# Kernel tuning notes

Hardware: AMD Instinct MI355X
Metric: run time of the kernel (lower is better)

Reference implementation:

```python
import jax, jax.numpy as jnp
import numpy as np

H = 64       # HIDDEN_DIM
HIST = 4     # HIST_LEN
V = 64       # VOCAB_SIZE
LSTM_H = 32  # trigger LSTM hidden size


def setup_inputs() -> dict:
    key = jax.random.key(0)
    ks = jax.random.split(key, 24)
    B, L, M = 1024, 256, 256
    s = 0.1

    def p(k, shape):
        return jax.random.normal(k, shape, dtype=jnp.float32) * s

    return {
        "seq": jax.random.randint(ks[0], (B, L), 0, V, dtype=jnp.int32),
        "memory": jax.random.normal(ks[1], (B, M, H), dtype=jnp.float32),
        # nn.Embedding(V, H)
        "embed_w": p(ks[2], (V, H)),
        # nn.GRUCell(2H, H): weight_ih (3H, 2H), weight_hh (3H, H)
        "gru_wih": p(ks[3], (3 * H, 2 * H)),
        "gru_whh": p(ks[4], (3 * H, H)),
        "gru_bih": p(ks[5], (3 * H,)),
        "gru_bhh": p(ks[6], (3 * H,)),
        # SoftAttentionMemory projections: Linear(H, H) each
        "q_w": p(ks[7], (H, H)), "q_b": p(ks[8], (H,)),
        "k_w": p(ks[9], (H, H)), "k_b": p(ks[10], (H,)),
        "v_w": p(ks[11], (H, H)), "v_b": p(ks[12], (H,)),
        # PredictiveTrigger nn.LSTM(H, 32): gate order i,f,g,o
        "lstm_wih": p(ks[13], (4 * LSTM_H, H)),
        "lstm_whh": p(ks[14], (4 * LSTM_H, LSTM_H)),
        "lstm_bih": p(ks[15], (4 * LSTM_H,)),
        "lstm_bhh": p(ks[16], (4 * LSTM_H,)),
        "trig_w": p(ks[17], (1, LSTM_H)), "trig_b": p(ks[18], (1,)),
        # output head Linear(H, V)
        "head_w": p(ks[19], (V, H)), "head_b": p(ks[20], (V,)),
    }


def reference(seq, memory, embed_w, gru_wih, gru_whh, gru_bih, gru_bhh,
              q_w, q_b, k_w, k_b, v_w, v_b,
              lstm_wih, lstm_whh, lstm_bih, lstm_bhh,
              trig_w, trig_b, head_w, head_b):
    B, L = seq.shape
    x_emb = embed_w[seq]                         # (B, L, H)
    # k/v projections of memory are time-invariant -> hoist out of the loop
    kmem = memory @ k_w.T + k_b                  # (B, M, H)
    vmem = memory @ v_w.T + v_b                  # (B, M, H)
    scale = 1.0 / jnp.sqrt(jnp.float32(H))

    def gru_cell(inp, h):
        gi = inp @ gru_wih.T + gru_bih           # (B, 3H)
        gh = h @ gru_whh.T + gru_bhh
        i_r, i_z, i_n = jnp.split(gi, 3, axis=-1)
        h_r, h_z, h_n = jnp.split(gh, 3, axis=-1)
        r = jax.nn.sigmoid(i_r + h_r)
        z = jax.nn.sigmoid(i_z + h_z)
        n = jnp.tanh(i_n + r * h_n)
        return (1.0 - z) * n + z * h

    def trigger(hist):                            # hist: (B, HIST, H) -> (B,)
        def lstm_step(carry, x_t):
            hh, cc = carry
            g = x_t @ lstm_wih.T + lstm_bih + hh @ lstm_whh.T + lstm_bhh
            i, f, gg, o = jnp.split(g, 4, axis=-1)
            cc = jax.nn.sigmoid(f) * cc + jax.nn.sigmoid(i) * jnp.tanh(gg)
            hh = jax.nn.sigmoid(o) * jnp.tanh(cc)
            return (hh, cc), None
        init = (jnp.zeros((hist.shape[0], LSTM_H), hist.dtype),
                jnp.zeros((hist.shape[0], LSTM_H), hist.dtype))
        (hh, _), _ = jax.lax.scan(lstm_step, init, jnp.swapaxes(hist, 0, 1))
        return jax.nn.sigmoid(hh @ trig_w.T + trig_b)[:, 0]

    def attend(h):                                # (B, H) -> (B, H)
        q = h @ q_w.T + q_b
        w = jax.nn.softmax(jnp.einsum('bh,bmh->bm', q, kmem) * scale, axis=-1)
        return jnp.einsum('bm,bmh->bh', w, vmem)

    def step(carry, xs):
        h, retrieved, hist, reads = carry
        x_t, t = xs
        h = gru_cell(jnp.concatenate([x_t, retrieved], axis=-1), h)
        # torch uses h.detach() for the trigger history
        hist = jnp.concatenate([hist[:, 1:], jax.lax.stop_gradient(h)[:, None]], axis=1)
        full = t >= HIST - 1                      # history buffer filled
        prob = trigger(hist)
        do_read = full & (jnp.mean(prob) > 0.5)
        retrieved = jnp.where(do_read, attend(h),
                              jnp.where(full, jnp.zeros_like(retrieved), retrieved))
        reads = reads + do_read.astype(jnp.float32)
        return (h, retrieved, hist, reads), None

    carry0 = (jnp.zeros((B, H), jnp.float32),
              jnp.zeros((B, H), jnp.float32),
              jnp.zeros((B, HIST, H), jnp.float32),
              jnp.float32(0.0))
    (h, _, _, reads), _ = jax.lax.scan(step, carry0,
                                       (jnp.swapaxes(x_emb, 0, 1), jnp.arange(L)))
    logits = h @ head_w.T + head_b               # (B, V)
    read_rate = reads / L
    return logits, read_rate
```

## Files before the change

kernel.cpp:

```cpp
#include <hip/hip_runtime.h>
#include <hip/hip_fp16.h>
#include <math.h>

#define OFF_TOKPROJ 0
#define OFF_ACC     12288
#define OFF_SLOT2   12800
#define OFF_HH      78336

#define THRESH30 (512ULL << 30)
#define THRESH27 (512ULL << 27)
#define SPIN_BOUND (1 << 18)

__device__ __forceinline__ float sigf(float x) {
    return __fdividef(1.f, 1.f + __expf(-x));
}
__device__ __forceinline__ float tanhf_fast(float x) {
    float e2 = __expf(-2.f * fabsf(x));
    float r = __fdividef(1.f - e2, 1.f + e2);
    return __uint_as_float(__float_as_uint(r) | (__float_as_uint(x) & 0x80000000u));
}

__device__ __forceinline__ unsigned int pack2(float x, float y) {
    union { unsigned int u; _Float16 h[2]; } v;
    v.h[0] = (_Float16)x; v.h[1] = (_Float16)y;
    return v.u;
}
__device__ __forceinline__ float unplo(unsigned int u) {
    union { unsigned int x; _Float16 h[2]; } v; v.x = u; return (float)v.h[0];
}
__device__ __forceinline__ float unphi(unsigned int u) {
    union { unsigned int x; _Float16 h[2]; } v; v.x = u; return (float)v.h[1];
}
__device__ __forceinline__ float dot2acc(unsigned int a, unsigned int b, float acc) {
#if __has_builtin(__builtin_amdgcn_fdot2)
    typedef _Float16 hf2 __attribute__((ext_vector_type(2)));
    union { unsigned int u; hf2 h; } ua, ub;
    ua.u = a; ub.u = b;
    return __builtin_amdgcn_fdot2(ua.h, ub.h, acc, false);
#else
    union { unsigned int u; _Float16 h[2]; } ua, ub;
    ua.u = a; ub.u = b;
    return acc + (float)ua.h[0] * (float)ub.h[0] + (float)ua.h[1] * (float)ub.h[1];
#endif
}

__global__ __launch_bounds__(64) void prep_k(
    const float* __restrict__ embed, const float* __restrict__ gwih,
    const float* __restrict__ gbih, float* __restrict__ ws)
{
    int blk = blockIdx.x, l = threadIdx.x;
    if (blk < 64) {
        float* tokproj = ws + OFF_TOKPROJ;
        int v = blk;
        for (int j = l; j < 192; j += 64) {
            float s = gbih[j];
            for (int d = 0; d < 64; ++d) s += embed[v * 64 + d] * gwih[j * 128 + d];
            tokproj[v * 192 + j] = s;
        }
    } else {
        float* z = ws + OFF_ACC;
        int base = (blk - 64) * 4096;
        int end = 512 + 65536;
        for (int i = base + l; i < base + 4096; i += 64)
            if (i < end) z[i] = 0.f;
    }
}

__global__ __launch_bounds__(256, 1) void gru_k(
    const int* __restrict__ seq, const float* __restrict__ gwhh,
    const float* __restrict__ gbhh, const float* __restrict__ hw,
    const float* __restrict__ hb, float* __restrict__ ws,
    float* __restrict__ out)
{
    int tid = threadIdx.x, w = tid >> 6, l = tid & 63, b = blockIdx.x;
    int r = b * 4 + w;
    const float* tokproj = ws + OFF_TOKPROJ;
    __half* Hh = (__half*)(ws + OFF_HH);

    __shared__ float hs[4][64];
    __shared__ int toks[4][256];
    for (int k = 0; k < 4; ++k) toks[w][k * 64 + l] = seq[r * 256 + k * 64 + l];

    float wh0[64], wh1[64], wh2[64];
    #pragma unroll
    for (int d4 = 0; d4 < 16; ++d4) {
        float4 a0 = *(const float4*)(gwhh + (size_t)l * 64 + d4 * 4);
        float4 a1 = *(const float4*)(gwhh + (size_t)(64 + l) * 64 + d4 * 4);
        float4 a2 = *(const float4*)(gwhh + (size_t)(128 + l) * 64 + d4 * 4);
        wh0[d4*4] = a0.x; wh0[d4*4+1] = a0.y; wh0[d4*4+2] = a0.z; wh0[d4*4+3] = a0.w;
        wh1[d4*4] = a1.x; wh1[d4*4+1] = a1.y; wh1[d4*4+2] = a1.z; wh1[d4*4+3] = a1.w;
        wh2[d4*4] = a2.x; wh2[d4*4+1] = a2.y; wh2[d4*4+2] = a2.z; wh2[d4*4+3] = a2.w;
    }
    float g0b = gbhh[l], g1b = gbhh[64 + l], g2b = gbhh[128 + l];

    float h = 0.f;
    hs[w][l] = 0.f;
    int tok0 = toks[w][0];
    float gi0 = tokproj[tok0 * 192 + l], gi1 = tokproj[tok0 * 192 + 64 + l],
          gi2 = tokproj[tok0 * 192 + 128 + l];

    for (int t = 0; t < 256; ++t) {
        float ni0 = 0.f, ni1 = 0.f, ni2 = 0.f;
        if (t < 255) {
            int tk = toks[w][t + 1];
            ni0 = tokproj[tk * 192 + l];
            ni1 = tokproj[tk * 192 + 64 + l];
            ni2 = tokproj[tk * 192 + 128 + l];
        }
        float A0[4] = {0.f, 0.f, 0.f, 0.f};
        float A1[4] = {0.f, 0.f, 0.f, 0.f};
        float A2[4] = {0.f, 0.f, 0.f, 0.f};
        #pragma unroll
        for (int d4 = 0; d4 < 16; ++d4) {
            float4 hv = *(const float4*)&hs[w][d4 * 4];
            A0[d4 & 3] += hv.x*wh0[d4*4] + hv.y*wh0[d4*4+1] + hv.z*wh0[d4*4+2] + hv.w*wh0[d4*4+3];
            A1[d4 & 3] += hv.x*wh1[d4*4] + hv.y*wh1[d4*4+1] + hv.z*wh1[d4*4+2] + hv.w*wh1[d4*4+3];
            A2[d4 & 3] += hv.x*wh2[d4*4] + hv.y*wh2[d4*4+1] + hv.z*wh2[d4*4+2] + hv.w*wh2[d4*4+3];
        }
        float gh0 = g0b + ((A0[0] + A0[1]) + (A0[2] + A0[3]));
        float gh1 = g1b + ((A1[0] + A1[1]) + (A1[2] + A1[3]));
        float gh2 = g2b + ((A2[0] + A2[1]) + (A2[2] + A2[3]));
        float r_ = sigf(gi0 + gh0), z_ = sigf(gi1 + gh1);
        float n_ = tanhf_fast(gi2 + r_ * gh2);
        h = (1.f - z_) * n_ + z_ * h;
        hs[w][l] = h;
        Hh[((size_t)r * 256 + t) * 64 + l] = __float2half(h);
        gi0 = ni0; gi1 = ni1; gi2 = ni2;
    }

    float sL = hb[l];
    #pragma unroll
    for (int d4 = 0; d4 < 16; ++d4) {
        float4 w4 = *(const float4*)(hw + (size_t)l * 64 + d4 * 4);
        float4 hv = *(const float4*)&hs[w][d4 * 4];
        sL += hv.x * w4.x + hv.y * w4.y + hv.z * w4.z + hv.w * w4.w;
    }
    out[r * 64 + l] = sL;
}

__global__ __launch_bounds__(256) void trig_k(
    const float* __restrict__ lwih, const float* __restrict__ lwhh,
    const float* __restrict__ lbih, const float* __restrict__ lbhh,
    const float* __restrict__ tw, const float* __restrict__ tb,
    float* __restrict__ ws)
{
    int tid = threadIdx.x, w = tid >> 6, l = tid & 63, b = blockIdx.x;
    int rg = b >> 4, c = b & 15;
    int r = rg * 4 + w;
    int t0 = 3 + 16 * c;
    int ntrig = (c == 15) ? 13 : 16;
    int wlen = ntrig + 3;

    const unsigned int* HhU = (const unsigned int*)(ws + OFF_HH);
    unsigned long long* acc = (unsigned long long*)(ws + OFF_ACC);

    __shared__ unsigned int hwin2[4][608];
    __shared__ unsigned int pwinp[4][19][64];
    __shared__ unsigned int hs2p[4][2][16];
    __shared__ unsigned int probq[4][16];

    unsigned int wl0h[32], wl1h[32], lh0h[16], lh1h[16];
    #pragma unroll
    for (int d2 = 0; d2 < 32; ++d2) {
        wl0h[d2] = pack2(lwih[(size_t)l * 64 + 2*d2], lwih[(size_t)l * 64 + 2*d2 + 1]);
        wl1h[d2] = pack2(lwih[(size_t)(64 + l) * 64 + 2*d2], lwih[(size_t)(64 + l) * 64 + 2*d2 + 1]);
    }
    #pragma unroll
    for (int d2 = 0; d2 < 16; ++d2) {
        lh0h[d2] = pack2(lwhh[(size_t)l * 32 + 2*d2], lwhh[(size_t)l * 32 + 2*d2 + 1]);
        lh1h[d2] = pack2(lwhh[(size_t)(64 + l) * 32 + 2*d2], lwhh[(size_t)(64 + l) * 32 + 2*d2 + 1]);
    }
    float lb0 = lbih[l] + lbhh[l], lb1 = lbih[64 + l] + lbhh[64 + l];
    float twr = (l < 32) ? tw[l] : 0.f;
    float tb0 = tb[0];

    for (int idx = l; idx < wlen * 32; idx += 64)
        hwin2[w][idx] = HhU[((size_t)r * 256 + (t0 - 3)) * 32 + idx];

    for (int i = 0; i < wlen; ++i) {
        float p0 = lb0, p1 = lb1;
        #pragma unroll
        for (int d8 = 0; d8 < 8; ++d8) {
            uint4 hv = *(const uint4*)&hwin2[w][i * 32 + d8 * 4];
            p0 = dot2acc(hv.x, wl0h[d8*4+0], p0); p1 = dot2acc(hv.x, wl1h[d8*4+0], p1);
            p0 = dot2acc(hv.y, wl0h[d8*4+1], p0); p1 = dot2acc(hv.y, wl1h[d8*4+1], p1);
            p0 = dot2acc(hv.z, wl0h[d8*4+2], p0); p1 = dot2acc(hv.z, wl1h[d8*4+2], p1);
            p0 = dot2acc(hv.w, wl0h[d8*4+3], p0); p1 = dot2acc(hv.w, wl1h[d8*4+3], p1);
        }
        pwinp[w][i][l] = pack2(p0, p1);
    }

    for (int jp = 0; jp < 8 && jp < ntrig; ++jp) {
        int ja = jp, jb = jp + 8;
        bool hasB = (jb < ntrig);
        float hhA = 0.f, ccA = 0.f, hhB = 0.f, ccB = 0.f;
        #pragma unroll
        for (int k = 0; k < 4; ++k) {
            unsigned int uA = pwinp[w][ja + k][l];
            float q0A = unplo(uA), q1A = unphi(uA);
            float q0B = 0.f, q1B = 0.f;
            if (hasB) {
                unsigned int uB = pwinp[w][jb + k][l];
                q0B = unplo(uB); q1B = unphi(uB);
            }
            if (k) {
                #pragma unroll
                for (int d4 = 0; d4 < 4; ++d4) {
                    uint4 ha = *(const uint4*)&hs2p[w][0][d4 * 4];
                    q0A = dot2acc(ha.x, lh0h[d4*4+0], q0A); q1A = dot2acc(ha.x, lh1h[d4*4+0], q1A);
                    q0A = dot2acc(ha.y, lh0h[d4*4+1], q0A); q1A = dot2acc(ha.y, lh1h[d4*4+1], q1A);
                    q0A = dot2acc(ha.z, lh0h[d4*4+2], q0A); q1A = dot2acc(ha.z, lh1h[d4*4+2], q1A);
                    q0A = dot2acc(ha.w, lh0h[d4*4+3], q0A); q1A = dot2acc(ha.w, lh1h[d4*4+3], q1A);
                }
                if (hasB) {
                    #pragma unroll
                    for (int d4 = 0; d4 < 4; ++d4) {
                        uint4 hb2 = *(const uint4*)&hs2p[w][1][d4 * 4];
                        q0B = dot2acc(hb2.x, lh0h[d4*4+0], q0B); q1B = dot2acc(hb2.x, lh1h[d4*4+0], q1B);
                        q0B = dot2acc(hb2.y, lh0h[d4*4+1], q0B); q1B = dot2acc(hb2.y, lh1h[d4*4+1], q1B);
                        q0B = dot2acc(hb2.z, lh0h[d4*4+2], q0B); q1B = dot2acc(hb2.z, lh1h[d4*4+2], q1B);
                        q0B = dot2acc(hb2.w, lh0h[d4*4+3], q0B); q1B = dot2acc(hb2.w, lh1h[d4*4+3], q1B);
                    }
                }
            }
            float s0A = sigf(q0A);
            float t1A = tanhf_fast(q1A);
            float s1A = sigf(q1A);
            float ffA = __shfl(s0A, l + 32);
            float ooA = __shfl(s1A, l + 32);
            float nccA = ffA * ccA + s0A * t1A;
            float nhA = ooA * tanhf_fast(nccA);
            if (l < 32) { ccA = nccA; hhA = nhA; }
            float nhB = 0.f;
            if (hasB) {
                float s0B = sigf(q0B);
                float t1B = tanhf_fast(q1B);
                float s1B = sigf(q1B);
                float ffB = __shfl(s0B, l + 32);
                float ooB = __shfl(s1B, l + 32);
                float nccB = ffB * ccB + s0B * t1B;
                nhB = ooB * tanhf_fast(nccB);
                if (l < 32) { ccB = nccB; hhB = nhB; }
            }
            if (k < 3) {
                float a0 = __shfl(nhA, 2 * l), a1 = __shfl(nhA, 2 * l + 1);
                if (l < 16) hs2p[w][0][l] = pack2(a0, a1);
                if (hasB) {
                    float b0 = __shfl(nhB, 2 * l), b1 = __shfl(nhB, 2 * l + 1);
                    if (l < 16) hs2p[w][1][l] = pack2(b0, b1);
                }
            }
        }
        float ppA = (l < 32) ? hhA * twr : 0.f;
        #pragma unroll
        for (int o = 32; o; o >>= 1) ppA += __shfl_xor(ppA, o);
        if (l == 0) {
            float prob = sigf(ppA + tb0);
            unsigned long long q = (unsigned long long)llrint((double)prob * 1073741824.0);
            if (q > 0x3FFFFFFFull) q = 0x3FFFFFFFull;
            probq[w][ja] = (unsigned int)q;
        }
        if (hasB) {
            float ppB = (l < 32) ? hhB * twr : 0.f;
            #pragma unroll
            for (int o = 32; o; o >>= 1) ppB += __shfl_xor(ppB, o);
            if (l == 0) {
                float prob = sigf(ppB + tb0);
                unsigned long long q = (unsigned long long)llrint((double)prob * 1073741824.0);
                if (q > 0x3FFFFFFFull) q = 0x3FFFFFFFull;
                probq[w][jb] = (unsigned int)q;
            }
        }
    }
    __syncthreads();
    if (w == 0 && l < ntrig) {
        unsigned int s = probq[0][l] + probq[1][l] + probq[2][l] + probq[3][l];
        atomicAdd(&acc[t0 + l], (unsigned long long)s);
    }
}

__global__ __launch_bounds__(256, 1) void fin_k(
    const int* __restrict__ seq, const float* __restrict__ memory,
    const float* __restrict__ gwih, const float* __restrict__ gwhh,
    const float* __restrict__ gbhh, const float* __restrict__ qw,
    const float* __restrict__ qb, const float* __restrict__ kw,
    const float* __restrict__ vw, const float* __restrict__ vb,
    const float* __restrict__ lwih, const float* __restrict__ lwhh,
    const float* __restrict__ lbih, const float* __restrict__ lbhh,
    const float* __restrict__ tw, const float* __restrict__ tb,
    const float* __restrict__ hw, const float* __restrict__ hb,
    float* __restrict__ ws, float* __restrict__ out)
{
    int tid = threadIdx.x, w = tid >> 6, l = tid & 63, b = blockIdx.x;
    const unsigned long long* acc = (const unsigned long long*)(ws + OFF_ACC);

    __shared__ int redmin[4];
    {
        int mymin = 1 << 30;
        if (tid >= 3 && acc[tid] > THRESH30) mymin = tid;
        #pragma unroll
        for (int o = 32; o; o >>= 1) mymin = min(mymin, __shfl_xor(mymin, o));
        if (l == 0) redmin[w] = mymin;
    }
    __syncthreads();
    int tc = min(min(redmin[0], redmin[1]), min(redmin[2], redmin[3]));
    if (tc > 255) {
        if (b == 0 && tid == 0) out[65536] = 0.f;
        return;
    }

    int r = b * 4 + w;
    const float* tokproj = ws + OFF_TOKPROJ;
    unsigned int* S2 = (unsigned int*)(ws + OFF_SLOT2);

    __shared__ float hs[4][64], qs[4][64], us[4][64], rs[4][64];
    __shared__ float hs2f[4][32];
    __shared__ float PXl[4][4][128];
    __shared__ unsigned int probq[4];
    __shared__ int flagLds;
    __shared__ int toks[4][256];

    for (int k = 0; k < 4; ++k) toks[w][k * 64 + l] = seq[r * 256 + k * 64 + l];
    if (tid == 0) flagLds = 0;

    float wh0[64], wh1[64], wh2[64], wl0[64], wl1[64], lh0[32], lh1[32];
    #pragma unroll
    for (int d4 = 0; d4 < 16; ++d4) {
        float4 a0 = *(const float4*)(gwhh + (size_t)l * 64 + d4 * 4);
        float4 a1 = *(const float4*)(gwhh + (size_t)(64 + l) * 64 + d4 * 4);
        float4 a2 = *(const float4*)(gwhh + (size_t)(128 + l) * 64 + d4 * 4);
        float4 b0 = *(const float4*)(lwih + (size_t)l * 64 + d4 * 4);
        float4 b1 = *(const float4*)(lwih + (size_t)(64 + l) * 64 + d4 * 4);
        wh0[d4*4] = a0.x; wh0[d4*4+1] = a0.y; wh0[d4*4+2] = a0.z; wh0[d4*4+3] = a0.w;
        wh1[d4*4] = a1.x; wh1[d4*4+1] = a1.y; wh1[d4*4+2] = a1.z; wh1[d4*4+3] = a1.w;
        wh2[d4*4] = a2.x; wh2[d4*4+1] = a2.y; wh2[d4*4+2] = a2.z; wh2[d4*4+3] = a2.w;
        wl0[d4*4] = b0.x; wl0[d4*4+1] = b0.y; wl0[d4*4+2] = b0.z; wl0[d4*4+3] = b0.w;
        wl1[d4*4] = b1.x; wl1[d4*4+1] = b1.y; wl1[d4*4+2] = b1.z; wl1[d4*4+3] = b1.w;
    }
    #pragma unroll
    for (int d4 = 0; d4 < 8; ++d4) {
        float4 c0 = *(const float4*)(lwhh + (size_t)l * 32 + d4 * 4);
        float4 c1 = *(const float4*)(lwhh + (size_t)(64 + l) * 32 + d4 * 4);
        lh0[d4*4] = c0.x; lh0[d4*4+1] = c0.y; lh0[d4*4+2] = c0.z; lh0[d4*4+3] = c0.w;
        lh1[d4*4] = c1.x; lh1[d4*4+1] = c1.y; lh1[d4*4+2] = c1.z; lh1[d4*4+3] = c1.w;
    }
    float g0b = gbhh[l], g1b = gbhh[64 + l], g2b = gbhh[128 + l];
    float lb0 = lbih[l] + lbhh[l], lb1 = lbih[64 + l] + lbhh[64 + l];
    float twr = (l < 32) ? tw[l] : 0.f;
    float tb0 = tb[0];
    const float* mrow = memory + (size_t)r * 16384;

    float h = 0.f;
    hs[w][l] = 0.f;
    bool fire = false, brk = false;
    int cnt = 1;
    __syncthreads();

    for (int t = 0; t < 256; ++t) {
        int tok = toks[w][t];
        float gi0 = tokproj[tok * 192 + l], gi1 = tokproj[tok * 192 + 64 + l],
              gi2 = tokproj[tok * 192 + 128 + l];
        float gh0 = g0b, gh1 = g1b, gh2 = g2b;
        #pragma unroll
        for (int d4 = 0; d4 < 16; ++d4) {
            float4 hv = *(const float4*)&hs[w][d4 * 4];
            gh0 += hv.x*wh0[d4*4] + hv.y*wh0[d4*4+1] + hv.z*wh0[d4*4+2] + hv.w*wh0[d4*4+3];
            gh1 += hv.x*wh1[d4*4] + hv.y*wh1[d4*4+1] + hv.z*wh1[d4*4+2] + hv.w*wh1[d4*4+3];
            gh2 += hv.x*wh2[d4*4] + hv.y*wh2[d4*4+1] + hv.z*wh2[d4*4+2] + hv.w*wh2[d4*4+3];
        }
        if (fire) {
            float q = qb[l];
            #pragma unroll
            for (int d4 = 0; d4 < 16; ++d4) {
                float4 q4 = *(const float4*)(qw + (size_t)l * 64 + d4 * 4);
                float4 hv = *(const float4*)&hs[w][d4 * 4];
                q += hv.x * q4.x + hv.y * q4.y + hv.z * q4.z + hv.w * q4.w;
            }
            qs[w][l] = q;
            float qk = 0.f;
            for (int e = 0; e < 64; ++e) qk += qs[w][e] * kw[(size_t)e * 64 + l];
            qk *= 0.125f;
            us[w][l] = qk;
            float sc[4];
            for (int k = 0; k < 4; ++k) {
                const float* mp = mrow + (size_t)(k * 64 + l) * 64;
                float s = 0.f;
                #pragma unroll
                for (int d4 = 0; d4 < 16; ++d4) {
                    float4 m4 = *(const float4*)(mp + d4 * 4);
                    float4 kv = *(const float4*)&us[w][d4 * 4];
                    s += m4.x * kv.x + m4.y * kv.y + m4.z * kv.z + m4.w * kv.w;
                }
                sc[k] = s;
            }
            float mx = fmaxf(fmaxf(sc[0], sc[1]), fmaxf(sc[2], sc[3]));
            for (int o = 32; o; o >>= 1) mx = fmaxf(mx, __shfl_xor(mx, o));
            float den = 0.f;
            #pragma unroll
            for (int k = 0; k < 4; ++k) { sc[k] = expf(sc[k] - mx); den += sc[k]; }
            for (int o = 32; o; o >>= 1) den += __shfl_xor(den, o);
            float u = 0.f;
            for (int m = 0; m < 256; ++m) {
                float wm = __shfl(sc[m >> 6], m & 63);
                u += wm * mrow[(size_t)m * 64 + l];
            }
            u /= den;
            us[w][l] = u;
            float ret = vb[l];
            #pragma unroll
            for (int d4 = 0; d4 < 16; ++d4) {
                float4 v4 = *(const float4*)(vw + (size_t)l * 64 + d4 * 4);
                float4 uv = *(const float4*)&us[w][d4 * 4];
                ret += uv.x * v4.x + uv.y * v4.y + uv.z * v4.z + uv.w * v4.w;
            }
            rs[w][l] = ret;
            for (int e = 0; e < 64; ++e) {
                float re = rs[w][e];
                gi0 += re * gwih[(size_t)l * 128 + 64 + e];
                gi1 += re * gwih[(size_t)(64 + l) * 128 + 64 + e];
                gi2 += re * gwih[(size_t)(128 + l) * 128 + 64 + e];
            }
        }
        fire = false;
        float r_ = sigf(gi0 + gh0), z_ = sigf(gi1 + gh1);
        float n_ = tanhf_fast(gi2 + r_ * gh2);
        h = (1.f - z_) * n_ + z_ * h;
        hs[w][l] = h;

        float p0 = lb0, p1 = lb1;
        #pragma unroll
        for (int d4 = 0; d4 < 16; ++d4) {
            float4 hv = *(const float4*)&hs[w][d4 * 4];
            p0 += hv.x*wl0[d4*4] + hv.y*wl0[d4*4+1] + hv.z*wl0[d4*4+2] + hv.w*wl0[d4*4+3];
            p1 += hv.x*wl1[d4*4] + hv.y*wl1[d4*4+1] + hv.z*wl1[d4*4+2] + hv.w*wl1[d4*4+3];
        }
        PXl[w][t & 3][l] = p0; PXl[w][t & 3][64 + l] = p1;

        if (t == tc) {
            fire = true;
        } else if (t > tc) {
            float hh = 0.f, cc = 0.f;
            #pragma unroll
            for (int k = 0; k < 4; ++k) {
                int s2 = (t - 3 + k) & 3;
                float q0 = PXl[w][s2][l], q1 = PXl[w][s2][64 + l];
                if (k) {
                    #pragma unroll
                    for (int d4 = 0; d4 < 8; ++d4) {
                        float4 hv = *(const float4*)&hs2f[w][d4 * 4];
                        q0 += hv.x*lh0[d4*4] + hv.y*lh0[d4*4+1] + hv.z*lh0[d4*4+2] + hv.w*lh0[d4*4+3];
                        q1 += hv.x*lh1[d4*4] + hv.y*lh1[d4*4+1] + hv.z*lh1[d4*4+2] + hv.w*lh1[d4*4+3];
                    }
                }
                float f_ = __shfl(q0, l + 32), o_ = __shfl(q1, l + 32);
                float ig = sigf(q0), ff = sigf(f_), gg = tanhf_fast(q1), oo = sigf(o_);
                float ncc = ff * cc + ig * gg;
                float nhh = oo * tanhf_fast(ncc);
                if (l < 32) { cc = ncc; hh = nhh; hs2f[w][l] = nhh; }
            }
            float pp = (l < 32) ? hh * twr : 0.f;
            #pragma unroll
            for (int o = 32; o; o >>= 1) pp += __shfl_xor(pp, o);
            if (l == 0) {
                float prob = sigf(pp + tb0);
                unsigned long long q = (unsigned long long)llrint((double)prob * 134217728.0);
                if (q > 0x7FFFFFFull) q = 0x7FFFFFFull;
                probq[w] = (unsigned int)q;
            }
            __syncthreads();
            if (w == 0 && l == 0) {
                unsigned int s = probq[0] + probq[1] + probq[2] + probq[3];
                __hip_atomic_store(&S2[(size_t)t * 256 + b], (1u << 30) | s,
                                   __ATOMIC_RELAXED, __HIP_MEMORY_SCOPE_AGENT);
            }
            if (w == 0) {
                unsigned long long tot = 0; int spin = 0; bool ok = true;
                if (!brk) {
                    for (;;) {
                        bool all4 = true; tot = 0;
                        #pragma unroll
                        for (int k2 = 0; k2 < 4; ++k2) {
                            unsigned int v = __hip_atomic_load(&S2[(size_t)t * 256 + k2 * 64 + l],
                                                               __ATOMIC_RELAXED, __HIP_MEMORY_SCOPE_AGENT);
                            all4 &= ((v >> 30) == 1u);
                            tot += (v & 0x3FFFFFFFu);
                        }
                        if (__all(all4)) break;
                        if (++spin > SPIN_BOUND) { ok = false; brk = true; break; }
                        __builtin_amdgcn_s_sleep(1);
                    }
                } else ok = false;
                #pragma unroll
                for (int o = 32; o; o >>= 1) tot += __shfl_xor(tot, o);
                int dec = (ok && tot > THRESH27) ? 1 : 0;
                cnt += dec;
                if (l == 0) flagLds = dec;
            }
            __syncthreads();
            fire = (flagLds != 0);
        }
    }

    float sL = hb[l];
    #pragma unroll
    for (int d4 = 0; d4 < 16; ++d4) {
        float4 w4 = *(const float4*)(hw + (size_t)l * 64 + d4 * 4);
        float4 hv = *(const float4*)&hs[w][d4 * 4];
        sL += hv.x * w4.x + hv.y * w4.y + hv.z * w4.z + hv.w * w4.w;
    }
    out[r * 64 + l] = sL;
    if (b == 0 && w == 0 && l == 0)
        out[65536] = brk ? -1234.f : (float)cnt / 256.f;
}

extern "C" void kernel_launch(void* const* d_in, const int* in_sizes, int n_in,
                              void* d_out, int out_size, void* d_ws, size_t ws_size,
                              hipStream_t stream)
{
    const int*   seq    = (const int*)d_in[0];
    const float* memory = (const float*)d_in[1];
    const float* embed  = (const float*)d_in[2];
    const float* gwih   = (const float*)d_in[3];
    const float* gwhh   = (const float*)d_in[4];
    const float* gbih   = (const float*)d_in[5];
    const float* gbhh   = (const float*)d_in[6];
    const float* qw     = (const float*)d_in[7];
    const float* qb     = (const float*)d_in[8];
    const float* kw     = (const float*)d_in[9];
    const float* vw     = (const float*)d_in[11];
    const float* vb     = (const float*)d_in[12];
    const float* lwih   = (const float*)d_in[13];
    const float* lwhh   = (const float*)d_in[14];
    const float* lbih   = (const float*)d_in[15];
    const float* lbhh   = (const float*)d_in[16];
    const float* tw     = (const float*)d_in[17];
    const float* tb     = (const float*)d_in[18];
    const float* hw     = (const float*)d_in[19];
    const float* hb     = (const float*)d_in[20];
    float* ws = (float*)d_ws;
    float* out = (float*)d_out;

    prep_k<<<81, 64, 0, stream>>>(embed, gwih, gbih, ws);
    gru_k<<<256, 256, 0, stream>>>(seq, gwhh, gbhh, hw, hb, ws, out);
    trig_k<<<4096, 256, 0, stream>>>(lwih, lwhh, lbih, lbhh, tw, tb, ws);
    fin_k<<<256, 256, 0, stream>>>(seq, memory, gwih, gwhh, gbhh, qw, qb, kw,
                                   vw, vb, lwih, lwhh, lbih, lbhh, tw, tb,
                                   hw, hb, ws, out);
}
```

Baseline: 548.4 us.

## Fuse GRU and trigger LSTM into one producer-consumer kernel with chunked handoff

Merges the GRU recurrence and the trigger-LSTM pass into one 512-thread kernel. Four waves run the GRU and write fp16 hidden states into a double-buffered shared chunk, while four other waves consume the previous chunk to compute trigger probabilities, synchronised per 16-step chunk. This removes the global fp16 hidden-state history round-trip and the separate 4096-block trigger launch, and replaces atomics with per-row slots reduced by a small kernel. The GRU recurrent matvec now uses fp16 dot2 with fp16-packed weights and state, which may change numerics. Per-chunk block barriers couple the two roles, so the trigger waves can stall the GRU.

```diff
diff --git a/kernel.cpp b/kernel.cpp
--- a/kernel.cpp
+++ b/kernel.cpp
@@ -5,7 +5,7 @@
 #define OFF_TOKPROJ 0
 #define OFF_ACC     12288
 #define OFF_SLOT2   12800
-#define OFF_HH      78336
+#define OFF_SLOTS   78336
 
 #define THRESH30 (512ULL << 30)
 #define THRESH27 (512ULL << 27)
@@ -19,7 +19,6 @@
     float r = __fdividef(1.f - e2, 1.f + e2);
     return __uint_as_float(__float_as_uint(r) | (__float_as_uint(x) & 0x80000000u));
 }
-
 __device__ __forceinline__ unsigned int pack2(float x, float y) {
     union { unsigned int u; _Float16 h[2]; } v;
     v.h[0] = (_Float16)x; v.h[1] = (_Float16)y;
@@ -58,225 +57,221 @@
             tokproj[v * 192 + j] = s;
         }
     } else {
-        float* z = ws + OFF_ACC;
+        float* z = ws + OFF_SLOT2;
         int base = (blk - 64) * 4096;
-        int end = 512 + 65536;
-        for (int i = base + l; i < base + 4096; i += 64)
-            if (i < end) z[i] = 0.f;
-    }
-}
-
-__global__ __launch_bounds__(256, 1) void gru_k(
+        for (int i = base + l; i < base + 4096; i += 64) z[i] = 0.f;
+    }
+}
+
+__global__ __launch_bounds__(512) void fused_k(
     const int* __restrict__ seq, const float* __restrict__ gwhh,
-    const float* __restrict__ gbhh, const float* __restrict__ hw,
+    const float* __restrict__ gbhh, const float* __restrict__ lwih,
+    const float* __restrict__ lwhh, const float* __restrict__ lbih,
+    const float* __restrict__ lbhh, const float* __restrict__ tw,
+    const float* __restrict__ tb, const float* __restrict__ hw,
     const float* __restrict__ hb, float* __restrict__ ws,
     float* __restrict__ out)
 {
     int tid = threadIdx.x, w = tid >> 6, l = tid & 63, b = blockIdx.x;
-    int r = b * 4 + w;
     const float* tokproj = ws + OFF_TOKPROJ;
-    __half* Hh = (__half*)(ws + OFF_HH);
-
-    __shared__ float hs[4][64];
-    __shared__ int toks[4][256];
-    for (int k = 0; k < 4; ++k) toks[w][k * 64 + l] = seq[r * 256 + k * 64 + l];
-
-    float wh0[64], wh1[64], wh2[64];
-    #pragma unroll
-    for (int d4 = 0; d4 < 16; ++d4) {
-        float4 a0 = *(const float4*)(gwhh + (size_t)l * 64 + d4 * 4);
-        float4 a1 = *(const float4*)(gwhh + (size_t)(64 + l) * 64 + d4 * 4);
-        float4 a2 = *(const float4*)(gwhh + (size_t)(128 + l) * 64 + d4 * 4);
-        wh0[d4*4] = a0.x; wh0[d4*4+1] = a0.y; wh0[d4*4+2] = a0.z; wh0[d4*4+3] = a0.w;
-        wh1[d4*4] = a1.x; wh1[d4*4+1] = a1.y; wh1[d4*4+2] = a1.z; wh1[d4*4+3] = a1.w;
-        wh2[d4*4] = a2.x; wh2[d4*4+1] = a2.y; wh2[d4*4+2] = a2.z; wh2[d4*4+3] = a2.w;
-    }
-    float g0b = gbhh[l], g1b = gbhh[64 + l], g2b = gbhh[128 + l];
-
-    float h = 0.f;
-    hs[w][l] = 0.f;
-    int tok0 = toks[w][0];
-    float gi0 = tokproj[tok0 * 192 + l], gi1 = tokproj[tok0 * 192 + 64 + l],
-          gi2 = tokproj[tok0 * 192 + 128 + l];
-
-    for (int t = 0; t < 256; ++t) {
-        float ni0 = 0.f, ni1 = 0.f, ni2 = 0.f;
-        if (t < 255) {
-            int tk = toks[w][t + 1];
-            ni0 = tokproj[tk * 192 + l];
-            ni1 = tokproj[tk * 192 + 64 + l];
-            ni2 = tokproj[tk * 192 + 128 + l];
-        }
-        float A0[4] = {0.f, 0.f, 0.f, 0.f};
-        float A1[4] = {0.f, 0.f, 0.f, 0.f};
-        float A2[4] = {0.f, 0.f, 0.f, 0.f};
-        #pragma unroll
-        for (int d4 = 0; d4 < 16; ++d4) {
-            float4 hv = *(const float4*)&hs[w][d4 * 4];
-            A0[d4 & 3] += hv.x*wh0[d4*4] + hv.y*wh0[d4*4+1] + hv.z*wh0[d4*4+2] + hv.w*wh0[d4*4+3];
-            A1[d4 & 3] += hv.x*wh1[d4*4] + hv.y*wh1[d4*4+1] + hv.z*wh1[d4*4+2] + hv.w*wh1[d4*4+3];
-            A2[d4 & 3] += hv.x*wh2[d4*4] + hv.y*wh2[d4*4+1] + hv.z*wh2[d4*4+2] + hv.w*wh2[d4*4+3];
-        }
-        float gh0 = g0b + ((A0[0] + A0[1]) + (A0[2] + A0[3]));
-        float gh1 = g1b + ((A1[0] + A1[1]) + (A1[2] + A1[3]));
-        float gh2 = g2b + ((A2[0] + A2[1]) + (A2[2] + A2[3]));
-        float r_ = sigf(gi0 + gh0), z_ = sigf(gi1 + gh1);
-        float n_ = tanhf_fast(gi2 + r_ * gh2);
-        h = (1.f - z_) * n_ + z_ * h;
-        hs[w][l] = h;
-        Hh[((size_t)r * 256 + t) * 64 + l] = __float2half(h);
-        gi0 = ni0; gi1 = ni1; gi2 = ni2;
-    }
-
-    float sL = hb[l];
-    #pragma unroll
-    for (int d4 = 0; d4 < 16; ++d4) {
-        float4 w4 = *(const float4*)(hw + (size_t)l * 64 + d4 * 4);
-        float4 hv = *(const float4*)&hs[w][d4 * 4];
-        sL += hv.x * w4.x + hv.y * w4.y + hv.z * w4.z + hv.w * w4.w;
-    }
-    out[r * 64 + l] = sL;
-}
-
-__global__ __launch_bounds__(256) void trig_k(
-    const float* __restrict__ lwih, const float* __restrict__ lwhh,
-    const float* __restrict__ lbih, const float* __restrict__ lbhh,
-    const float* __restrict__ tw, const float* __restrict__ tb,
-    float* __restrict__ ws)
-{
-    int tid = threadIdx.x, w = tid >> 6, l = tid & 63, b = blockIdx.x;
-    int rg = b >> 4, c = b & 15;
-    int r = rg * 4 + w;
-    int t0 = 3 + 16 * c;
-    int ntrig = (c == 15) ? 13 : 16;
-    int wlen = ntrig + 3;
-
-    const unsigned int* HhU = (const unsigned int*)(ws + OFF_HH);
-    unsigned long long* acc = (unsigned long long*)(ws + OFF_ACC);
-
-    __shared__ unsigned int hwin2[4][608];
+    unsigned int* slots = (unsigned int*)(ws + OFF_SLOTS);
+
+    __shared__ unsigned int hbuf[4][2][19][32];
     __shared__ unsigned int pwinp[4][19][64];
     __shared__ unsigned int hs2p[4][2][16];
-    __shared__ unsigned int probq[4][16];
-
-    unsigned int wl0h[32], wl1h[32], lh0h[16], lh1h[16];
+    __shared__ int toks[4][256];
+
+    for (int i = tid; i < 1024; i += 512) toks[i >> 8][i & 255] = seq[(size_t)b * 1024 + i];
+    __syncthreads();
+
+    if (w < 4) {
+        int r = b * 4 + w;
+        unsigned int wh0h[32], wh1h[32], wh2h[32];
+        #pragma unroll
+        for (int d2 = 0; d2 < 32; ++d2) {
+            wh0h[d2] = pack2(gwhh[(size_t)l * 64 + 2*d2], gwhh[(size_t)l * 64 + 2*d2 + 1]);
+            wh1h[d2] = pack2(gwhh[(size_t)(64 + l) * 64 + 2*d2], gwhh[(size_t)(64 + l) * 64 + 2*d2 + 1]);
+            wh2h[d2] = pack2(gwhh[(size_t)(128 + l) * 64 + 2*d2], gwhh[(size_t)(128 + l) * 64 + 2*d2 + 1]);
+        }
+        float g0b = gbhh[l], g1b = gbhh[64 + l], g2b = gbhh[128 + l];
+        float h = 0.f;
+        if (l < 32) { hbuf[w][0][0][l] = 0u; hbuf[w][0][1][l] = 0u; hbuf[w][0][2][l] = 0u; }
+        int tok0 = toks[w][0];
+        float gi0 = tokproj[tok0 * 192 + l], gi1 = tokproj[tok0 * 192 + 64 + l],
+              gi2 = tokproj[tok0 * 192 + 128 + l];
+
+        for (int c = 0; c < 16; ++c) {
+            int cb = c & 1;
+            if (c > 0 && l < 32) {
+                hbuf[w][cb][0][l] = hbuf[w][cb ^ 1][16][l];
+                hbuf[w][cb][1][l] = hbuf[w][cb ^ 1][17][l];
+                hbuf[w][cb][2][l] = hbuf[w][cb ^ 1][18][l];
+            }
+            for (int s = 0; s < 16; ++s) {
+                int t = c * 16 + s;
+                float ni0 = 0.f, ni1 = 0.f, ni2 = 0.f;
+                if (t < 255) {
+                    int tk = toks[w][t + 1];
+                    ni0 = tokproj[tk * 192 + l];
+                    ni1 = tokproj[tk * 192 + 64 + l];
+                    ni2 = tokproj[tk * 192 + 128 + l];
+                }
+                float A00 = 0.f, A01 = 0.f, A10 = 0.f, A11 = 0.f, A20 = 0.f, A21 = 0.f;
+                #pragma unroll
+                for (int d8 = 0; d8 < 8; ++d8) {
+                    uint4 hv = *(const uint4*)&hbuf[w][cb][s + 2][d8 * 4];
+                    A00 = dot2acc(hv.x, wh0h[d8*4+0], A00); A01 = dot2acc(hv.y, wh0h[d8*4+1], A01);
+                    A00 = dot2acc(hv.z, wh0h[d8*4+2], A00); A01 = dot2acc(hv.w, wh0h[d8*4+3], A01);
+                    A10 = dot2acc(hv.x, wh1h[d8*4+0], A10); A11 = dot2acc(hv.y, wh1h[d8*4+1], A11);
+                    A10 = dot2acc(hv.z, wh1h[d8*4+2], A10); A11 = dot2acc(hv.w, wh1h[d8*4+3], A11);
+                    A20 = dot2acc(hv.x, wh2h[d8*4+0], A20); A21 = dot2acc(hv.y, wh2h[d8*4+1], A21);
+                    A20 = dot2acc(hv.z, wh2h[d8*4+2], A20); A21 = dot2acc(hv.w, wh2h[d8*4+3], A21);
+                }
+                float gh0 = g0b + A00 + A01;
+                float gh1 = g1b + A10 + A11;
+                float gh2 = g2b + A20 + A21;
+                float r_ = sigf(gi0 + gh0), z_ = sigf(gi1 + gh1);
+                float n_ = tanhf_fast(gi2 + r_ * gh2);
+                h = (1.f - z_) * n_ + z_ * h;
+                float a0 = __shfl(h, 2 * l), a1 = __shfl(h, 2 * l + 1);
+                if (l < 32) hbuf[w][cb][s + 3][l] = pack2(a0, a1);
+                gi0 = ni0; gi1 = ni1; gi2 = ni2;
+            }
+            __syncthreads();
+        }
+        float sL = hb[l];
+        #pragma unroll
+        for (int d4 = 0; d4 < 16; ++d4) {
+            float4 w4 = *(const float4*)(hw + (size_t)l * 64 + d4 * 4);
+            unsigned int h0 = hbuf[w][1][18][d4 * 2], h1 = hbuf[w][1][18][d4 * 2 + 1];
+            sL += unplo(h0) * w4.x + unphi(h0) * w4.y + unplo(h1) * w4.z + unphi(h1) * w4.w;
+        }
+        out[r * 64 + l] = sL;
+    } else {
+        int rw = w - 4;
+        int r = b * 4 + rw;
+        unsigned int wl0h[32], wl1h[32], lh0h[16], lh1h[16];
+        #pragma unroll
+        for (int d2 = 0; d2 < 32; ++d2) {
+            wl0h[d2] = pack2(lwih[(size_t)l * 64 + 2*d2], lwih[(size_t)l * 64 + 2*d2 + 1]);
+            wl1h[d2] = pack2(lwih[(size_t)(64 + l) * 64 + 2*d2], lwih[(size_t)(64 + l) * 64 + 2*d2 + 1]);
+        }
+        #pragma unroll
+        for (int d2 = 0; d2 < 16; ++d2) {
+            lh0h[d2] = pack2(lwhh[(size_t)l * 32 + 2*d2], lwhh[(size_t)l * 32 + 2*d2 + 1]);
+            lh1h[d2] = pack2(lwhh[(size_t)(64 + l) * 32 + 2*d2], lwhh[(size_t)(64 + l) * 32 + 2*d2 + 1]);
+        }
+        float lb0 = lbih[l] + lbhh[l], lb1 = lbih[64 + l] + lbhh[64 + l];
+        float twr = (l < 32) ? tw[l] : 0.f;
+        float tb0 = tb[0];
+
+        auto do_chunk = [&](int cc) {
+            int bb = cc & 1, base = cc * 16;
+            for (int i = 0; i < 19; ++i) {
+                float p0 = lb0, p1 = lb1;
+                #pragma unroll
+                for (int d8 = 0; d8 < 8; ++d8) {
+                    uint4 hv = *(const uint4*)&hbuf[rw][bb][i][d8 * 4];
+                    p0 = dot2acc(hv.x, wl0h[d8*4+0], p0); p1 = dot2acc(hv.x, wl1h[d8*4+0], p1);
+                    p0 = dot2acc(hv.y, wl0h[d8*4+1], p0); p1 = dot2acc(hv.y, wl1h[d8*4+1], p1);
+                    p0 = dot2acc(hv.z, wl0h[d8*4+2], p0); p1 = dot2acc(hv.z, wl1h[d8*4+2], p1);
+                    p0 = dot2acc(hv.w, wl0h[d8*4+3], p0); p1 = dot2acc(hv.w, wl1h[d8*4+3], p1);
+                }
+                pwinp[rw][i][l] = pack2(p0, p1);
+            }
+            for (int jp = 0; jp < 8; ++jp) {
+                int ja = jp, jb2 = jp + 8;
+                bool hasA = (base + ja >= 3);
+                float hhA = 0.f, ccA = 0.f, hhB = 0.f, ccB = 0.f;
+                #pragma unroll
+                for (int k = 0; k < 4; ++k) {
+                    unsigned int uA = pwinp[rw][ja + k][l];
+                    float q0A = unplo(uA), q1A = unphi(uA);
+                    unsigned int uB = pwinp[rw][jb2 + k][l];
+                    float q0B = unplo(uB), q1B = unphi(uB);
+                    if (k) {
+                        #pragma unroll
+                        for (int d4 = 0; d4 < 4; ++d4) {
+                            uint4 ha = *(const uint4*)&hs2p[rw][0][d4 * 4];
+                            q0A = dot2acc(ha.x, lh0h[d4*4+0], q0A); q1A = dot2acc(ha.x, lh1h[d4*4+0], q1A);
+                            q0A = dot2acc(ha.y, lh0h[d4*4+1], q0A); q1A = dot2acc(ha.y, lh1h[d4*4+1], q1A);
+                            q0A = dot2acc(ha.z, lh0h[d4*4+2], q0A); q1A = dot2acc(ha.z, lh1h[d4*4+2], q1A);
+                            q0A = dot2acc(ha.w, lh0h[d4*4+3], q0A); q1A = dot2acc(ha.w, lh1h[d4*4+3], q1A);
+                        }
+                        #pragma unroll
+                        for (int d4 = 0; d4 < 4; ++d4) {
+                            uint4 hb2 = *(const uint4*)&hs2p[rw][1][d4 * 4];
+                            q0B = dot2acc(hb2.x, lh0h[d4*4+0], q0B); q1B = dot2acc(hb2.x, lh1h[d4*4+0], q1B);
+                            q0B = dot2acc(hb2.y, lh0h[d4*4+1], q0B); q1B = dot2acc(hb2.y, lh1h[d4*4+1], q1B);
+                            q0B = dot2acc(hb2.z, lh0h[d4*4+2], q0B); q1B = dot2acc(hb2.z, lh1h[d4*4+2], q1B);
+                            q0B = dot2acc(hb2.w, lh0h[d4*4+3], q0B); q1B = dot2acc(hb2.w, lh1h[d4*4+3], q1B);
+                        }
+                    }
+                    float s0A = sigf(q0A);
+                    float t1A = tanhf_fast(q1A);
+                    float s1A = sigf(q1A);
+                    float ffA = __shfl(s0A, l + 32);
+                    float ooA = __shfl(s1A, l + 32);
+                    float nccA = ffA * ccA + s0A * t1A;
+                    float nhA = ooA * tanhf_fast(nccA);
+                    if (l < 32) { ccA = nccA; hhA = nhA; }
+                    float s0B = sigf(q0B);
+                    float t1B = tanhf_fast(q1B);
+                    float s1B = sigf(q1B);
+                    float ffB = __shfl(s0B, l + 32);
+                    float ooB = __shfl(s1B, l + 32);
+                    float nccB = ffB * ccB + s0B * t1B;
+                    float nhB = ooB * tanhf_fast(nccB);
+                    if (l < 32) { ccB = nccB; hhB = nhB; }
+                    if (k < 3) {
+                        float a0 = __shfl(nhA, 2 * l), a1 = __shfl(nhA, 2 * l + 1);
+                        if (l < 16) hs2p[rw][0][l] = pack2(a0, a1);
+                        float b0 = __shfl(nhB, 2 * l), b1 = __shfl(nhB, 2 * l + 1);
+                        if (l < 16) hs2p[rw][1][l] = pack2(b0, b1);
+                    }
+                }
+                float ppA = (l < 32) ? hhA * twr : 0.f;
+                #pragma unroll
+                for (int o = 32; o; o >>= 1) ppA += __shfl_xor(ppA, o);
+                if (hasA && l == 0) {
+                    float prob = sigf(ppA + tb0);
+                    unsigned long long q = (unsigned long long)llrint((double)prob * 1073741824.0);
+                    if (q > 0x3FFFFFFFull) q = 0x3FFFFFFFull;
+                    slots[(size_t)(base + ja) * 1024 + r] = (unsigned int)q;
+                }
+                float ppB = (l < 32) ? hhB * twr : 0.f;
+                #pragma unroll
+                for (int o = 32; o; o >>= 1) ppB += __shfl_xor(ppB, o);
+                if (l == 0) {
+                    float prob = sigf(ppB + tb0);
+                    unsigned long long q = (unsigned long long)llrint((double)prob * 1073741824.0);
+                    if (q > 0x3FFFFFFFull) q = 0x3FFFFFFFull;
+                    slots[(size_t)(base + jb2) * 1024 + r] = (unsigned int)q;
+                }
+            }
+        };
+
+        for (int c = 0; c < 16; ++c) {
+            if (c > 0) do_chunk(c - 1);
+            __syncthreads();
+        }
+        do_chunk(15);
+    }
+}
+
+__global__ __launch_bounds__(256) void red_k(float* __restrict__ ws)
+{
+    int tid = threadIdx.x, w = tid >> 6, l = tid & 63;
+    int t = 3 + blockIdx.x * 4 + w;
+    if (t > 255) return;
+    const unsigned int* slots = (const unsigned int*)(ws + OFF_SLOTS);
+    unsigned long long* acc = (unsigned long long*)(ws + OFF_ACC);
+    unsigned long long s = 0;
     #pragma unroll
-    for (int d2 = 0; d2 < 32; ++d2) {
-        wl0h[d2] = pack2(lwih[(size_t)l * 64 + 2*d2], lwih[(size_t)l * 64 + 2*d2 + 1]);
-        wl1h[d2] = pack2(lwih[(size_t)(64 + l) * 64 + 2*d2], lwih[(size_t)(64 + l) * 64 + 2*d2 + 1]);
-    }
+    for (int k = 0; k < 16; ++k) s += slots[(size_t)t * 1024 + k * 64 + l];
     #pragma unroll
-    for (int d2 = 0; d2 < 16; ++d2) {
-        lh0h[d2] = pack2(lwhh[(size_t)l * 32 + 2*d2], lwhh[(size_t)l * 32 + 2*d2 + 1]);
-        lh1h[d2] = pack2(lwhh[(size_t)(64 + l) * 32 + 2*d2], lwhh[(size_t)(64 + l) * 32 + 2*d2 + 1]);
-    }
-    float lb0 = lbih[l] + lbhh[l], lb1 = lbih[64 + l] + lbhh[64 + l];
-    float twr = (l < 32) ? tw[l] : 0.f;
-    float tb0 = tb[0];
-
-    for (int idx = l; idx < wlen * 32; idx += 64)
-        hwin2[w][idx] = HhU[((size_t)r * 256 + (t0 - 3)) * 32 + idx];
-
-    for (int i = 0; i < wlen; ++i) {
-        float p0 = lb0, p1 = lb1;
-        #pragma unroll
-        for (int d8 = 0; d8 < 8; ++d8) {
-            uint4 hv = *(const uint4*)&hwin2[w][i * 32 + d8 * 4];
-            p0 = dot2acc(hv.x, wl0h[d8*4+0], p0); p1 = dot2acc(hv.x, wl1h[d8*4+0], p1);
-            p0 = dot2acc(hv.y, wl0h[d8*4+1], p0); p1 = dot2acc(hv.y, wl1h[d8*4+1], p1);
-            p0 = dot2acc(hv.z, wl0h[d8*4+2], p0); p1 = dot2acc(hv.z, wl1h[d8*4+2], p1);
-            p0 = dot2acc(hv.w, wl0h[d8*4+3], p0); p1 = dot2acc(hv.w, wl1h[d8*4+3], p1);
-        }
-        pwinp[w][i][l] = pack2(p0, p1);
-    }
-
-    for (int jp = 0; jp < 8 && jp < ntrig; ++jp) {
-        int ja = jp, jb = jp + 8;
-        bool hasB = (jb < ntrig);
-        float hhA = 0.f, ccA = 0.f, hhB = 0.f, ccB = 0.f;
-        #pragma unroll
-        for (int k = 0; k < 4; ++k) {
-            unsigned int uA = pwinp[w][ja + k][l];
-            float q0A = unplo(uA), q1A = unphi(uA);
-            float q0B = 0.f, q1B = 0.f;
-            if (hasB) {
-                unsigned int uB = pwinp[w][jb + k][l];
-                q0B = unplo(uB); q1B = unphi(uB);
-            }
-            if (k) {
-                #pragma unroll
-                for (int d4 = 0; d4 < 4; ++d4) {
-                    uint4 ha = *(const uint4*)&hs2p[w][0][d4 * 4];
-                    q0A = dot2acc(ha.x, lh0h[d4*4+0], q0A); q1A = dot2acc(ha.x, lh1h[d4*4+0], q1A);
-                    q0A = dot2acc(ha.y, lh0h[d4*4+1], q0A); q1A = dot2acc(ha.y, lh1h[d4*4+1], q1A);
-                    q0A = dot2acc(ha.z, lh0h[d4*4+2], q0A); q1A = dot2acc(ha.z, lh1h[d4*4+2], q1A);
-                    q0A = dot2acc(ha.w, lh0h[d4*4+3], q0A); q1A = dot2acc(ha.w, lh1h[d4*4+3], q1A);
-                }
-                if (hasB) {
-                    #pragma unroll
-                    for (int d4 = 0; d4 < 4; ++d4) {
-                        uint4 hb2 = *(const uint4*)&hs2p[w][1][d4 * 4];
-                        q0B = dot2acc(hb2.x, lh0h[d4*4+0], q0B); q1B = dot2acc(hb2.x, lh1h[d4*4+0], q1B);
-                        q0B = dot2acc(hb2.y, lh0h[d4*4+1], q0B); q1B = dot2acc(hb2.y, lh1h[d4*4+1], q1B);
-                        q0B = dot2acc(hb2.z, lh0h[d4*4+2], q0B); q1B = dot2acc(hb2.z, lh1h[d4*4+2], q1B);
-                        q0B = dot2acc(hb2.w, lh0h[d4*4+3], q0B); q1B = dot2acc(hb2.w, lh1h[d4*4+3], q1B);
-                    }
-                }
-            }
-            float s0A = sigf(q0A);
-            float t1A = tanhf_fast(q1A);
-            float s1A = sigf(q1A);
-            float ffA = __shfl(s0A, l + 32);
-            float ooA = __shfl(s1A, l + 32);
-            float nccA = ffA * ccA + s0A * t1A;
-            float nhA = ooA * tanhf_fast(nccA);
-            if (l < 32) { ccA = nccA; hhA = nhA; }
-            float nhB = 0.f;
-            if (hasB) {
-                float s0B = sigf(q0B);
-                float t1B = tanhf_fast(q1B);
-                float s1B = sigf(q1B);
-                float ffB = __shfl(s0B, l + 32);
-                float ooB = __shfl(s1B, l + 32);
-                float nccB = ffB * ccB + s0B * t1B;
-                nhB = ooB * tanhf_fast(nccB);
-                if (l < 32) { ccB = nccB; hhB = nhB; }
-            }
-            if (k < 3) {
-                float a0 = __shfl(nhA, 2 * l), a1 = __shfl(nhA, 2 * l + 1);
-                if (l < 16) hs2p[w][0][l] = pack2(a0, a1);
-                if (hasB) {
-                    float b0 = __shfl(nhB, 2 * l), b1 = __shfl(nhB, 2 * l + 1);
-                    if (l < 16) hs2p[w][1][l] = pack2(b0, b1);
-                }
-            }
-        }
-        float ppA = (l < 32) ? hhA * twr : 0.f;
-        #pragma unroll
-        for (int o = 32; o; o >>= 1) ppA += __shfl_xor(ppA, o);
-        if (l == 0) {
-            float prob = sigf(ppA + tb0);
-            unsigned long long q = (unsigned long long)llrint((double)prob * 1073741824.0);
-            if (q > 0x3FFFFFFFull) q = 0x3FFFFFFFull;
-            probq[w][ja] = (unsigned int)q;
-        }
-        if (hasB) {
-            float ppB = (l < 32) ? hhB * twr : 0.f;
-            #pragma unroll
-            for (int o = 32; o; o >>= 1) ppB += __shfl_xor(ppB, o);
-            if (l == 0) {
-                float prob = sigf(ppB + tb0);
-                unsigned long long q = (unsigned long long)llrint((double)prob * 1073741824.0);
-                if (q > 0x3FFFFFFFull) q = 0x3FFFFFFFull;
-                probq[w][jb] = (unsigned int)q;
-            }
-        }
-    }
-    __syncthreads();
-    if (w == 0 && l < ntrig) {
-        unsigned int s = probq[0][l] + probq[1][l] + probq[2][l] + probq[3][l];
-        atomicAdd(&acc[t0 + l], (unsigned long long)s);
-    }
+    for (int o = 32; o; o >>= 1) s += __shfl_xor(s, o);
+    if (l == 0) acc[t] = s;
 }
 
 __global__ __launch_bounds__(256, 1) void fin_k(
@@ -540,9 +535,10 @@
     float* ws = (float*)d_ws;
     float* out = (float*)d_out;
 
-    prep_k<<<81, 64, 0, stream>>>(embed, gwih, gbih, ws);
-    gru_k<<<256, 256, 0, stream>>>(seq, gwhh, gbhh, hw, hb, ws, out);
-    trig_k<<<4096, 256, 0, stream>>>(lwih, lwhh, lbih, lbhh, tw, tb, ws);
+    prep_k<<<80, 64, 0, stream>>>(embed, gwih, gbih, ws);
+    fused_k<<<256, 512, 0, stream>>>(seq, gwhh, gbhh, lwih, lwhh, lbih, lbhh,
+                                     tw, tb, hw, hb, ws, out);
+    red_k<<<64, 256, 0, stream>>>(ws);
     fin_k<<<256, 256, 0, stream>>>(seq, memory, gwih, gwhh, gbhh, qw, qb, kw,
                                    vw, vb, lwih, lwhh, lbih, lbhh, tw, tb,
                                    hw, hb, ws, out);
```

New measurement: 509.3 us. 7.1% less time.
